# Optimization experiments

Measured on AMD Instinct MI355X. Metric: run time of the kernel, lower is better.

Reference implementation:

```python
import jax, jax.numpy as jnp
import numpy as np

B, C, H, W = 32, 256, 7, 7
HEADS = 8
DIM_HEAD = 64
INNER = HEADS * DIM_HEAD  # 512
N_ANGLES = 16
KS = 5
GROUPS = 32
EPS = 1e-5


def setup_inputs() -> dict:
    key = jax.random.key(0)
    ks = jax.random.split(key, 16)
    w = lambda k, shp: jax.random.normal(k, shp, jnp.float32) * 0.05
    return {
        'x': jax.random.normal(ks[0], (B, C, H, W), jnp.float32),
        'gn_g': jnp.ones((C,), jnp.float32), 'gn_b': jnp.zeros((C,), jnp.float32),
        'sa_w1': w(ks[1], (C // 8, C)), 'sa_b1': jnp.zeros((C // 8,), jnp.float32),
        'sa_w2': w(ks[2], (C, C // 8)), 'sa_b2': jnp.zeros((C,), jnp.float32),
        'sa_gn_g': jnp.ones((C,), jnp.float32), 'sa_gn_b': jnp.zeros((C,), jnp.float32),
        'ra_gn_g': jnp.ones((C,), jnp.float32), 'ra_gn_b': jnp.zeros((C,), jnp.float32),
        'ra_qkv_w': w(ks[3], (3 * C, C)),
        'ra_proj_w': w(ks[4], (C, C)), 'ra_proj_b': jnp.zeros((C,), jnp.float32),
        'aa_ln_g': jnp.ones((C,), jnp.float32), 'aa_ln_b': jnp.zeros((C,), jnp.float32),
        'aa_qkv_w': w(ks[5], (3 * INNER, C)),
        'aa_relpos': w(ks[6], (2 * 7 - 1, 2 * 7 - 1, HEADS)),
        'aa_out_w': w(ks[7], (C, INNER)), 'aa_out_b': jnp.zeros((C,), jnp.float32),
        'ad_dir_w': w(ks[8], (N_ANGLES, C, C, KS, KS)),
        'ad_ap_w1': w(ks[9], (128, C)), 'ad_ap_b1': jnp.zeros((128,), jnp.float32),
        'ad_ap_w2': w(ks[10], (N_ANGLES, 128)), 'ad_ap_b2': jnp.zeros((N_ANGLES,), jnp.float32),
        'ad_proj_w': w(ks[11], (C, C)), 'ad_proj_b': jnp.zeros((C,), jnp.float32),
        'gate_w': w(ks[12], (4, C)), 'gate_b': jnp.zeros((4,), jnp.float32),
        'proj_w': w(ks[13], (C, C)), 'proj_b': jnp.zeros((C,), jnp.float32),
    }


def _gn(x, g, b):
    Bx, Cx, Hx, Wx = x.shape
    xr = x.reshape(Bx, GROUPS, -1)
    m = xr.mean(-1, keepdims=True)
    v = xr.var(-1, keepdims=True)
    xn = ((xr - m) * jax.lax.rsqrt(v + EPS)).reshape(Bx, Cx, Hx, Wx)
    return xn * g[None, :, None, None] + b[None, :, None, None]


def _c1(x, w, b=None):
    y = jnp.einsum('bchw,oc->bohw', x, w)
    return y if b is None else y + b[None, :, None, None]


def _rot_attn_pass(x, qkv_w):
    Bx, Cx, Hx, Wx = x.shape
    d = Cx // HEADS
    q, k, v = jnp.split(_c1(x, qkv_w), 3, axis=1)
    sh = lambda t: t.reshape(Bx, HEADS, d, Hx * Wx).transpose(0, 1, 3, 2)  # b h n d
    q, k, v = sh(q), sh(k), sh(v)
    a = jax.nn.softmax(jnp.einsum('bhid,bhjd->bhij', q, k) * (d ** -0.5), axis=-1)
    o = jnp.einsum('bhij,bhjd->bhid', a, v)
    return o.transpose(0, 1, 3, 2).reshape(Bx, Cx, Hx, Wx)


def _forward(x, gn_g, gn_b, sa_w1, sa_b1, sa_w2, sa_b2, sa_gn_g, sa_gn_b,
             ra_gn_g, ra_gn_b, ra_qkv_w, ra_proj_w, ra_proj_b,
             aa_ln_g, aa_ln_b, aa_qkv_w, aa_relpos, aa_out_w, aa_out_b,
             ad_dir_w, ad_ap_w1, ad_ap_b1, ad_ap_w2, ad_ap_b2, ad_proj_w, ad_proj_b,
             gate_w, gate_b, proj_w, proj_b):
    normed = _gn(x, gn_g, gn_b)

    # --- SpatialAttention branch ---
    wts = jax.nn.sigmoid(_c1(jax.nn.relu(_c1(normed, sa_w1, sa_b1)), sa_w2, sa_b2))
    spatial = _gn(normed * wts + normed, sa_gn_g, sa_gn_b)

    # --- RotationAwareAttention branch: 4 rot90 passes, max-fused ---
    xr = _gn(normed, ra_gn_g, ra_gn_b)
    r0 = _rot_attn_pass(xr, ra_qkv_w)
    r1 = jnp.rot90(_rot_attn_pass(jnp.rot90(xr, 1, (2, 3)), ra_qkv_w), 3, (2, 3))
    r2 = jnp.rot90(_rot_attn_pass(jnp.rot90(xr, 2, (2, 3)), ra_qkv_w), 2, (2, 3))
    r3 = jnp.rot90(_rot_attn_pass(jnp.rot90(xr, 3, (2, 3)), ra_qkv_w), 1, (2, 3))
    mx = jnp.maximum(jnp.maximum(r0, r1), jnp.maximum(r2, r3))
    rotation = _c1(mx, ra_proj_w, ra_proj_b) + normed

    # --- AngleAwareSelfAttention branch (rel-pos-biased MHSA over 49 tokens) ---
    Nn = H * W
    t = normed.reshape(B, C, Nn).transpose(0, 2, 1)  # [B,N,C]
    mu = t.mean(-1, keepdims=True)
    var = t.var(-1, keepdims=True)
    tn = (t - mu) * jax.lax.rsqrt(var + EPS) * aa_ln_g + aa_ln_b
    q, k, v = jnp.split(jnp.einsum('bnc,oc->bno', tn, aa_qkv_w), 3, axis=-1)
    sh = lambda u: u.reshape(B, Nn, HEADS, DIM_HEAD).transpose(0, 2, 1, 3)
    q, k, v = sh(q), sh(k), sh(v)
    dots = jnp.einsum('bhid,bhjd->bhij', q, k) * (DIM_HEAD ** -0.5)
    idx = jnp.arange(Nn)
    yi, xi = idx // W, idx % W
    dy = yi[None, :] - yi[:, None] + (H - 1)  # offsets into 13x13 table
    dx = xi[None, :] - xi[:, None] + (W - 1)
    bias = aa_relpos[dy, dx].transpose(2, 0, 1)[None]  # [1,heads,N,N]
    attn = jax.nn.softmax(dots + bias, axis=-1)
    o = jnp.einsum('bhij,bhjd->bhid', attn, v).transpose(0, 2, 1, 3).reshape(B, Nn, INNER)
    o = jnp.einsum('bni,oi->bno', o, aa_out_w) + aa_out_b
    angle = o.transpose(0, 2, 1).reshape(B, C, H, W) + normed

    # --- AngleAdaptiveAttention branch: 16 directional 5x5 convs + learned softmax gate ---
    dir_out = jax.lax.conv_general_dilated(
        normed, ad_dir_w.reshape(N_ANGLES * C, C, KS, KS), (1, 1), 'SAME',
        dimension_numbers=('NCHW', 'OIHW', 'NCHW')).reshape(B, N_ANGLES, C, H, W)
    gap = normed.mean((2, 3))  # [B,C]
    h1 = jax.nn.relu(gap @ ad_ap_w1.T + ad_ap_b1)
    aw = jax.nn.softmax(h1 @ ad_ap_w2.T + ad_ap_b2, axis=1)  # [B,16]
    comb = jnp.einsum('bkchw,bk->bchw', dir_out, aw)
    adaptive = _c1(comb, ad_proj_w, ad_proj_b) + normed

    # --- gated fusion ---
    gates = jax.nn.softmax(_c1(x, gate_w, gate_b), axis=1)  # [B,4,H,W]
    fused = (spatial * gates[:, 0:1] + rotation * gates[:, 1:2]
             + angle * gates[:, 2:3] + adaptive * gates[:, 3:4])
    return _c1(fused, proj_w, proj_b) + x


def reference(x, gn_g, gn_b, sa_w1, sa_b1, sa_w2, sa_b2, sa_gn_g, sa_gn_b,
              ra_gn_g, ra_gn_b, ra_qkv_w, ra_proj_w, ra_proj_b,
              aa_ln_g, aa_ln_b, aa_qkv_w, aa_relpos, aa_out_w, aa_out_b,
              ad_dir_w, ad_ap_w1, ad_ap_b1, ad_ap_w2, ad_ap_b2, ad_proj_w, ad_proj_b,
              gate_w, gate_b, proj_w, proj_b):
    return _forward(x, gn_g, gn_b, sa_w1, sa_b1, sa_w2, sa_b2, sa_gn_g, sa_gn_b,
                    ra_gn_g, ra_gn_b, ra_qkv_w, ra_proj_w, ra_proj_b,
                    aa_ln_g, aa_ln_b, aa_qkv_w, aa_relpos, aa_out_w, aa_out_b,
                    ad_dir_w, ad_ap_w1, ad_ap_b1, ad_ap_w2, ad_ap_b2, ad_proj_w, ad_proj_b,
                    gate_w, gate_b, proj_w, proj_b)
```

## Files before the change

kernel.cpp:

```cpp
#include <hip/hip_runtime.h>

#define EPS 1e-5f
typedef unsigned short u16;
typedef unsigned int u32;
typedef float f32x4 __attribute__((ext_vector_type(4)));
typedef short bf16x8 __attribute__((ext_vector_type(8)));

__device__ __forceinline__ float bf2f(u16 h){
  return __uint_as_float(((u32)h) << 16);
}
__device__ __forceinline__ u16 f2bf(float f){
  u32 u = __float_as_uint(f);
  u += 0x7fffu + ((u >> 16) & 1u);
  return (u16)(u >> 16);
}
__device__ __forceinline__ u32 pk2(float lo, float hi){
  return ((u32)f2bf(hi) << 16) | (u32)f2bf(lo);
}
union BF8 { bf16x8 v; u32 u[4]; };

__global__ __launch_bounds__(256) void k_prep1(
    const float* __restrict__ x, const float* __restrict__ gn_g, const float* __restrict__ gn_b,
    const float* __restrict__ ra_g, const float* __restrict__ ra_b,
    float* __restrict__ normed, float* __restrict__ xr, float* __restrict__ gap)
{
  int ch = blockIdx.x, b = blockIdx.y;
  int c0 = ch * 32;
  __shared__ float xs[1568], ns[1568];
  const float* xb = x + ((size_t)b * 256 + c0) * 49;
  for (int i = threadIdx.x; i < 1568; i += 256) xs[i] = xb[i];
  __syncthreads();
  int wv = threadIdx.x >> 6, lane = threadIdx.x & 63;
  const float* gsrc = xs + wv * 392;
  float* ndst = ns + wv * 392;
  float s = 0.f, ss = 0.f;
  for (int i = lane; i < 392; i += 64){ float v = gsrc[i]; s += v; ss += v * v; }
  for (int off = 32; off; off >>= 1){ s += __shfl_down(s, off); ss += __shfl_down(ss, off); }
  s = __shfl(s, 0); ss = __shfl(ss, 0);
  float m = s / 392.f, rs = rsqrtf(ss / 392.f - m * m + EPS);
  for (int i = lane; i < 392; i += 64){
    int c = c0 + wv * 8 + i / 49;
    ndst[i] = (gsrc[i] - m) * rs * gn_g[c] + gn_b[c];
  }
  __syncthreads();
  float* nb = normed + ((size_t)b * 256 + c0) * 49;
  for (int i = threadIdx.x; i < 1568; i += 256) nb[i] = ns[i];
  if (threadIdx.x < 32){
    float g2 = 0.f; const float* rp = ns + threadIdx.x * 49;
    for (int p = 0; p < 49; p++) g2 += rp[p];
    gap[(size_t)b * 256 + c0 + threadIdx.x] = g2 * (1.f / 49.f);
  }
  s = 0.f; ss = 0.f;
  for (int i = lane; i < 392; i += 64){ float v = ndst[i]; s += v; ss += v * v; }
  for (int off = 32; off; off >>= 1){ s += __shfl_down(s, off); ss += __shfl_down(ss, off); }
  s = __shfl(s, 0); ss = __shfl(ss, 0);
  m = s / 392.f; rs = rsqrtf(ss / 392.f - m * m + EPS);
  float* xrb = xr + ((size_t)b * 256 + c0) * 49;
  for (int i = lane; i < 392; i += 64){
    int c = c0 + wv * 8 + i / 49;
    xrb[wv * 392 + i] = (ndst[i] - m) * rs * ra_g[c] + ra_b[c];
  }
}

__global__ __launch_bounds__(256) void k_pos(
    const float* __restrict__ x, const float* __restrict__ normed,
    const float* __restrict__ gate_w, const float* __restrict__ gate_b,
    float* __restrict__ gates_g, float* __restrict__ lnm_g, float* __restrict__ lnr_g)
{
  int pc = blockIdx.x, b = blockIdx.y;
  __shared__ float gw[1024];
  for (int i = threadIdx.x; i < 1024; i += 256) gw[i] = gate_w[i];
  __syncthreads();
  int wv = threadIdx.x >> 6, lane = threadIdx.x & 63;
  for (int pi = wv; pi < 7; pi += 4){
    int p = pc * 7 + pi;
    const float* nb = normed + (size_t)b * 12544 + p;
    const float* xb = x + (size_t)b * 12544 + p;
    float s = 0.f, ss = 0.f, g0 = 0.f, g1 = 0.f, g2 = 0.f, g3 = 0.f;
    for (int c = lane; c < 256; c += 64){
      float nv = nb[c * 49];
      float xv = xb[c * 49];
      s += nv; ss += nv * nv;
      g0 += xv * gw[c]; g1 += xv * gw[256 + c];
      g2 += xv * gw[512 + c]; g3 += xv * gw[768 + c];
    }
    for (int off = 32; off; off >>= 1){
      s += __shfl_down(s, off); ss += __shfl_down(ss, off);
      g0 += __shfl_down(g0, off); g1 += __shfl_down(g1, off);
      g2 += __shfl_down(g2, off); g3 += __shfl_down(g3, off);
    }
    if (lane == 0){
      float mu = s / 256.f;
      lnm_g[b * 49 + p] = mu;
      lnr_g[b * 49 + p] = rsqrtf(ss / 256.f - mu * mu + EPS);
      g0 += gate_b[0]; g1 += gate_b[1]; g2 += gate_b[2]; g3 += gate_b[3];
      float mx = fmaxf(fmaxf(g0, g1), fmaxf(g2, g3));
      float e0 = __expf(g0 - mx), e1 = __expf(g1 - mx), e2 = __expf(g2 - mx), e3 = __expf(g3 - mx);
      float inv = 1.f / (e0 + e1 + e2 + e3);
      float* gg = gates_g + (size_t)b * 196 + p;
      gg[0] = e0 * inv; gg[49] = e1 * inv; gg[98] = e2 * inv; gg[147] = e3 * inv;
    }
  }
}

__global__ __launch_bounds__(256) void k_h1aw(
    const float* __restrict__ normed, const float* __restrict__ sa_w1, const float* __restrict__ sa_b1,
    const float* __restrict__ ap_w1, const float* __restrict__ ap_b1,
    const float* __restrict__ ap_w2, const float* __restrict__ ap_b2,
    const float* __restrict__ gap_g,
    float* __restrict__ h1_g, float* __restrict__ aw_g)
{
  int xb2 = blockIdx.x, b = blockIdx.y;
  int t = threadIdx.x;
  if (xb2 == 7){
    __shared__ float gaps[256], h[128], lg[16];
    gaps[t] = gap_g[b * 256 + t];
    __syncthreads();
    if (t < 128){
      float s = ap_b1[t];
      const float* wr = ap_w1 + t * 256;
      #pragma unroll 4
      for (int c = 0; c < 256; c++) s += gaps[c] * wr[c];
      h[t] = fmaxf(s, 0.f);
    }
    __syncthreads();
    if (t < 16){
      float s = ap_b2[t];
      const float* wr = ap_w2 + t * 128;
      #pragma unroll 4
      for (int o = 0; o < 128; o++) s += h[o] * wr[o];
      lg[t] = s;
    }
    __syncthreads();
    if (t == 0){
      float mx = -1e30f;
      for (int k = 0; k < 16; k++) mx = fmaxf(mx, lg[k]);
      float e[16], sm = 0.f;
      for (int k = 0; k < 16; k++){ e[k] = __expf(lg[k] - mx); sm += e[k]; }
      float inv = 1.f / sm;
      for (int k = 0; k < 16; k++) aw_g[b * 16 + k] = e[k] * inv;
    }
    return;
  }
  __shared__ float w1t[256 * 33];
  __shared__ float ns2[256 * 7];
  int p0 = xb2 * 7;
  for (int i = t; i < 8192; i += 256){
    int o = i >> 8, c = i & 255;
    w1t[c * 33 + o] = sa_w1[i];
  }
  for (int i = t; i < 1792; i += 256){
    int c = i / 7, pl = i - c * 7;
    ns2[i] = normed[(size_t)b * 12544 + c * 49 + p0 + pl];
  }
  __syncthreads();
  if (t < 224){
    int pl = t >> 5, o = t & 31;
    float s = sa_b1[o];
    #pragma unroll 8
    for (int c = 0; c < 256; c++) s += ns2[c * 7 + pl] * w1t[c * 33 + o];
    h1_g[(size_t)b * 1568 + (p0 + pl) * 32 + o] = fmaxf(s, 0.f);
  }
}

__global__ __launch_bounds__(256) void k_spatial(
    const float* __restrict__ normed, const float* __restrict__ h1_g,
    const float* __restrict__ sa_w2, const float* __restrict__ sa_b2,
    const float* __restrict__ sa_g, const float* __restrict__ sa_bb,
    float* __restrict__ spat_g)
{
  int gc = blockIdx.x, b = blockIdx.y;
  __shared__ float h1s[49 * 33];
  __shared__ float w2s[1024];
  int t = threadIdx.x;
  for (int i = t; i < 1568; i += 256){
    int p = i >> 5, o = i & 31;
    h1s[p * 33 + o] = h1_g[(size_t)b * 1568 + i];
  }
  for (int i = t; i < 1024; i += 256) w2s[i] = sa_w2[gc * 1024 + i];
  __syncthreads();
  int wv = t >> 6, lane = t & 63;
  int cg0 = wv * 8;
  const float* nb = normed + (size_t)b * 12544 + (gc * 32 + cg0) * 49;
  float tmp[7];
  float s = 0.f, ss = 0.f;
  #pragma unroll
  for (int j = 0; j < 7; j++){
    int i = lane + 64 * j;
    float v = 0.f;
    if (i < 392){
      int c = i / 49;
      const float* wr = w2s + (cg0 + c) * 32;
      const float* hp = h1s + (i - c * 49) * 33;
      float d = sa_b2[gc * 32 + cg0 + c];
      #pragma unroll
      for (int o = 0; o < 32; o++) d += hp[o] * wr[o];
      v = nb[i] * (1.f + 1.f / (1.f + __expf(-d)));
      s += v; ss += v * v;
    }
    tmp[j] = v;
  }
  for (int off = 32; off; off >>= 1){ s += __shfl_down(s, off); ss += __shfl_down(ss, off); }
  s = __shfl(s, 0); ss = __shfl(ss, 0);
  float m = s / 392.f, rs = rsqrtf(ss / 392.f - m * m + EPS);
  float* sb = spat_g + (size_t)b * 12544 + (gc * 32 + cg0) * 49;
  #pragma unroll
  for (int j = 0; j < 7; j++){
    int i = lane + 64 * j;
    if (i < 392){
      int c = gc * 32 + cg0 + i / 49;
      sb[i] = (tmp[j] - m) * rs * sa_g[c] + sa_bb[c];
    }
  }
}

__global__ __launch_bounds__(256) void k_weff(
    const float* __restrict__ W, const float* __restrict__ aw, u16* __restrict__ weff)
{
  const size_t t = ((size_t)blockIdx.x * 256 + threadIdx.x) * 2;
  const size_t CS = 819200;
  float2 A[16], B[16];
  #pragma unroll
  for (int k = 0; k < 16; k++) A[k] = *(const float2*)(W + (size_t)k * 1638400 + t);
  #pragma unroll
  for (int k = 0; k < 16; k++) B[k] = *(const float2*)(W + (size_t)k * 1638400 + t + CS);

  #pragma unroll 1
  for (int b = 0; b < 32; b++){
    float s0 = 0.f, s1 = 0.f;
    #pragma unroll
    for (int k = 0; k < 16; k++){
      float a = aw[b * 16 + k];
      s0 += a * A[k].x; s1 += a * A[k].y;
    }
    __builtin_nontemporal_store(pk2(s0, s1), (u32*)(weff + (size_t)b * 1638400 + t));
  }
  #pragma unroll 1
  for (int b = 0; b < 32; b++){
    float s0 = 0.f, s1 = 0.f;
    #pragma unroll
    for (int k = 0; k < 16; k++){
      float a = aw[b * 16 + k];
      s0 += a * B[k].x; s1 += a * B[k].y;
    }
    __builtin_nontemporal_store(pk2(s0, s1), (u32*)(weff + (size_t)b * 1638400 + t + CS));
  }
}

__global__ __launch_bounds__(256) void k_im2col(
    const float* __restrict__ normed, u16* __restrict__ xim)
{
  int p = blockIdx.x, b = blockIdx.y;
  __shared__ u16 row[6400];
  int ci = threadIdx.x;
  int py = p / 7, px = p - py * 7;
  const float* nb = normed + (size_t)b * 12544 + ci * 49;
  u16* rp = row + ci * 25;
  #pragma unroll
  for (int sy = 0; sy < 5; sy++){
    int iy = py + sy - 2;
    #pragma unroll
    for (int sx = 0; sx < 5; sx++){
      int ix = px + sx - 2;
      float v = (iy >= 0 && iy < 7 && ix >= 0 && ix < 7) ? nb[iy * 7 + ix] : 0.f;
      rp[sy * 5 + sx] = f2bf(v);
    }
  }
  __syncthreads();
  const u32* rs = (const u32*)row;
  u32* od = (u32*)(xim + (size_t)(b * 49 + p) * 6400);
  for (int i = threadIdx.x; i < 3200; i += 256) od[i] = rs[i];
}

__global__ __launch_bounds__(256) void k_conv_mfma(
    const u16* __restrict__ weff, const u16* __restrict__ xim, float* __restrict__ partial)
{
  int bx = blockIdx.x, b = blockIdx.y;
  int mblk = bx >> 3, kp = bx & 7;
  int wv = threadIdx.x >> 6, lane = threadIdx.x & 63;
  int lo = lane & 15, hi = lane >> 4;
  int co0 = mblk * 128 + wv * 32;
  const u16* wr0 = weff + (size_t)b * 1638400 + (size_t)(co0 + lo) * 6400 + kp * 800 + hi * 8;
  const u16* wr1 = wr0 + 16 * 6400;
  const u16* xb = xim + (size_t)b * 313600 + (size_t)lo * 6400 + kp * 800 + hi * 8;
  f32x4 acc[2][4];
  #pragma unroll
  for (int mi = 0; mi < 2; mi++)
    #pragma unroll
    for (int pi = 0; pi < 4; pi++) acc[mi][pi] = (f32x4){0.f, 0.f, 0.f, 0.f};
  #pragma unroll 1
  for (int ks = 0; ks < 25; ks++){
    int k0 = ks * 32;
    bf16x8 A0 = *(const bf16x8*)(wr0 + k0);
    bf16x8 A1 = *(const bf16x8*)(wr1 + k0);
    bf16x8 B0 = *(const bf16x8*)(xb + k0);
    bf16x8 B1 = *(const bf16x8*)(xb + 16 * 6400 + k0);
    bf16x8 B2 = *(const bf16x8*)(xb + 32 * 6400 + k0);
    bf16x8 B3 = *(const bf16x8*)(xb + 48 * 6400 + k0);
    acc[0][0] = __builtin_amdgcn_mfma_f32_16x16x32_bf16(A0, B0, acc[0][0], 0, 0, 0);
    acc[0][1] = __builtin_amdgcn_mfma_f32_16x16x32_bf16(A0, B1, acc[0][1], 0, 0, 0);
    acc[0][2] = __builtin_amdgcn_mfma_f32_16x16x32_bf16(A0, B2, acc[0][2], 0, 0, 0);
    acc[0][3] = __builtin_amdgcn_mfma_f32_16x16x32_bf16(A0, B3, acc[0][3], 0, 0, 0);
    acc[1][0] = __builtin_amdgcn_mfma_f32_16x16x32_bf16(A1, B0, acc[1][0], 0, 0, 0);
    acc[1][1] = __builtin_amdgcn_mfma_f32_16x16x32_bf16(A1, B1, acc[1][1], 0, 0, 0);
    acc[1][2] = __builtin_amdgcn_mfma_f32_16x16x32_bf16(A1, B2, acc[1][2], 0, 0, 0);
    acc[1][3] = __builtin_amdgcn_mfma_f32_16x16x32_bf16(A1, B3, acc[1][3], 0, 0, 0);
  }
  float* pb = partial + ((size_t)kp * 32 + b) * 12544;
  #pragma unroll
  for (int mi = 0; mi < 2; mi++){
    #pragma unroll
    for (int pi = 0; pi < 4; pi++){
      int p = pi * 16 + lo;
      if (p < 49){
        #pragma unroll
        for (int r = 0; r < 4; r++){
          int co = co0 + mi * 16 + hi * 4 + r;
          pb[co * 49 + p] = acc[mi][pi][r];
        }
      }
    }
  }
}

__global__ __launch_bounds__(256) void k_conv_reduce(
    const float* __restrict__ part, float* __restrict__ comb)
{
  int i = blockIdx.x * 256 + threadIdx.x;
  if (i >= 100352) return;
  float a0 = 0.f, a1 = 0.f, a2 = 0.f, a3 = 0.f;
  #pragma unroll
  for (int p = 0; p < 8; p++){
    float4 v = ((const float4*)part)[(size_t)p * 100352 + i];
    a0 += v.x; a1 += v.y; a2 += v.z; a3 += v.w;
  }
  float4 o; o.x = a0; o.y = a1; o.z = a2; o.w = a3;
  ((float4*)comb)[i] = o;
}

__device__ __forceinline__ void mfma_gemm_dev(
    const float* __restrict__ W, const float* __restrict__ bias,
    const float* __restrict__ act, const float* __restrict__ res,
    float* __restrict__ out, int M, int K, int m0blk, int p0, int b,
    const float* __restrict__ lnm, const float* __restrict__ lnr,
    const float* __restrict__ lng, const float* __restrict__ lnb)
{
  int wv = threadIdx.x >> 6, lane = threadIdx.x & 63;
  int lo = lane & 15, hi = lane >> 4;
  int m0 = m0blk + wv * 32;
  int p = p0 + lo;
  bool pok = p < 49;
  const float* ab = act + (size_t)b * K * 49;
  float lm = 0.f, lr = 0.f;
  if (lng && pok){ lm = lnm[p]; lr = lnr[p]; }
  f32x4 acc0 = {0.f, 0.f, 0.f, 0.f};
  f32x4 acc1 = {0.f, 0.f, 0.f, 0.f};
  const float* wr0 = W + (size_t)(m0 + lo) * K + hi * 8;
  const float* wr1 = W + (size_t)(m0 + 16 + lo) * K + hi * 8;
  for (int k0 = 0; k0 < K; k0 += 32){
    int kb = k0 + hi * 8;
    float4 a0lo = *(const float4*)(wr0 + k0);
    float4 a0hi = *(const float4*)(wr0 + k0 + 4);
    float4 a1lo = *(const float4*)(wr1 + k0);
    float4 a1hi = *(const float4*)(wr1 + k0 + 4);
    float bv[8];
    if (pok){
      const float* ap = ab + (size_t)kb * 49 + p;
      #pragma unroll
      for (int i = 0; i < 8; i++) bv[i] = ap[i * 49];
      if (lng){
// ... 1 lines not shown
        for (int i = 0; i < 8; i++) bv[i] = (bv[i] - lm) * lr * lng[kb + i] + lnb[kb + i];
      }
    } else {
      #pragma unroll
      for (int i = 0; i < 8; i++) bv[i] = 0.f;
    }
    BF8 A0, A1, B;
    A0.u[0] = pk2(a0lo.x, a0lo.y); A0.u[1] = pk2(a0lo.z, a0lo.w);
    A0.u[2] = pk2(a0hi.x, a0hi.y); A0.u[3] = pk2(a0hi.z, a0hi.w);
    A1.u[0] = pk2(a1lo.x, a1lo.y); A1.u[1] = pk2(a1lo.z, a1lo.w);
    A1.u[2] = pk2(a1hi.x, a1hi.y); A1.u[3] = pk2(a1hi.z, a1hi.w);
    B.u[0] = pk2(bv[0], bv[1]); B.u[1] = pk2(bv[2], bv[3]);
    B.u[2] = pk2(bv[4], bv[5]); B.u[3] = pk2(bv[6], bv[7]);
    acc0 = __builtin_amdgcn_mfma_f32_16x16x32_bf16(A0.v, B.v, acc0, 0, 0, 0);
    acc1 = __builtin_amdgcn_mfma_f32_16x16x32_bf16(A1.v, B.v, acc1, 0, 0, 0);
  }
  if (pok){
    #pragma unroll
    for (int r = 0; r < 4; r++){
      int m = m0 + hi * 4 + r;
      size_t idx = ((size_t)b * M + m) * 49 + p;
      float v = acc0[r] + (bias ? bias[m] : 0.f);
      if (res) v += res[idx];
      out[idx] = v;
      int m2 = m + 16;
      size_t idx2 = idx + 16 * 49;
      float v2 = acc1[r] + (bias ? bias[m2] : 0.f);
      if (res) v2 += res[idx2];
      out[idx2] = v2;
    }
  }
}

__global__ __launch_bounds__(256) void k_qkv(
    const float* __restrict__ ra_w, const float* __restrict__ aa_w,
    const float* __restrict__ xr, const float* __restrict__ normed,
    const float* __restrict__ lnm, const float* __restrict__ lnr,
    const float* __restrict__ ln_g, const float* __restrict__ ln_b,
    float* __restrict__ ra_qkv, float* __restrict__ aa_qkv)
{
  int bx = blockIdx.x, b = blockIdx.y;
  if (bx < 24){
    int m0 = (bx >> 2) * 128, p0 = (bx & 3) * 16;
    mfma_gemm_dev(ra_w, nullptr, xr, nullptr, ra_qkv, 768, 256, m0, p0, b,
                  nullptr, nullptr, nullptr, nullptr);
  } else {
    int bx2 = bx - 24;
    int m0 = (bx2 >> 2) * 128, p0 = (bx2 & 3) * 16;
    mfma_gemm_dev(aa_w, nullptr, normed, nullptr, aa_qkv, 1536, 256, m0, p0, b,
                  lnm + b * 49, lnr + b * 49, ln_g, ln_b);
  }
}

__global__ __launch_bounds__(256) void k_proj3(
    const float* __restrict__ ra_pw, const float* __restrict__ ra_pb, const float* __restrict__ r0,
    const float* __restrict__ aa_ow, const float* __restrict__ aa_ob, const float* __restrict__ aa_o,
    const float* __restrict__ ad_pw, const float* __restrict__ ad_pb, const float* __restrict__ comb,
    const float* __restrict__ normed,
    float* __restrict__ rotf, float* __restrict__ angf, float* __restrict__ adpf)
{
  int bx = blockIdx.x, b = blockIdx.y;
  if (bx < 8){
    int m0 = (bx >> 2) * 128, p0 = (bx & 3) * 16;
    mfma_gemm_dev(ra_pw, ra_pb, r0, normed, rotf, 256, 256, m0, p0, b,
                  nullptr, nullptr, nullptr, nullptr);
  } else if (bx < 16){
    int bx2 = bx - 8;
    int m0 = (bx2 >> 2) * 128, p0 = (bx2 & 3) * 16;
    mfma_gemm_dev(aa_ow, aa_ob, aa_o, normed, angf, 256, 512, m0, p0, b,
                  nullptr, nullptr, nullptr, nullptr);
  } else {
    int bx2 = bx - 16;
    int m0 = (bx2 >> 2) * 128, p0 = (bx2 & 3) * 16;
    mfma_gemm_dev(ad_pw, ad_pb, comb, normed, adpf, 256, 256, m0, p0, b,
                  nullptr, nullptr, nullptr, nullptr);
  }
}

__global__ __launch_bounds__(256) void k_final(
    const float* __restrict__ proj_w, const float* __restrict__ proj_b,
    const float* __restrict__ spat, const float* __restrict__ rotf,
    const float* __restrict__ angf, const float* __restrict__ adpf,
    const float* __restrict__ gates, const float* __restrict__ x,
    float* __restrict__ out)
// ... 22 lines not shown
    float4 a1lo = *(const float4*)(wr1 + k0);
    float4 a1hi = *(const float4*)(wr1 + k0 + 4);
    float bv[8];
    if (pok){
      size_t base = boff + (size_t)kb * 49 + p;
      #pragma unroll
      for (int i = 0; i < 8; i++){
        size_t idx = base + (size_t)i * 49;
        bv[i] = spat[idx] * g0 + rotf[idx] * g1 + angf[idx] * g2 + adpf[idx] * g3;
      }
    } else {
      #pragma unroll
      for (int i = 0; i < 8; i++) bv[i] = 0.f;
    }
    BF8 A0, A1, B;
    A0.u[0] = pk2(a0lo.x, a0lo.y); A0.u[1] = pk2(a0lo.z, a0lo.w);
    A0.u[2] = pk2(a0hi.x, a0hi.y); A0.u[3] = pk2(a0hi.z, a0hi.w);
    A1.u[0] = pk2(a1lo.x, a1lo.y); A1.u[1] = pk2(a1lo.z, a1lo.w);
    A1.u[2] = pk2(a1hi.x, a1hi.y); A1.u[3] = pk2(a1hi.z, a1hi.w);
    B.u[0] = pk2(bv[0], bv[1]); B.u[1] = pk2(bv[2], bv[3]);
    B.u[2] = pk2(bv[4], bv[5]); B.u[3] = pk2(bv[6], bv[7]);
    acc0 = __builtin_amdgcn_mfma_f32_16x16x32_bf16(A0.v, B.v, acc0, 0, 0, 0);
    acc1 = __builtin_amdgcn_mfma_f32_16x16x32_bf16(A1.v, B.v, acc1, 0, 0, 0);
  }
  if (pok){
    #pragma unroll
    for (int r = 0; r < 4; r++){
      int m = m0 + hi * 4 + r;
      size_t idx = boff + (size_t)m * 49 + p;
      out[idx] = acc0[r] + proj_b[m] + x[idx];
      int m2 = m + 16;
      size_t idx2 = idx + 16 * 49;
      out[idx2] = acc1[r] + proj_b[m2] + x[idx2];
    }
  }
}

__device__ __forceinline__ void softmax_rows(float* sc, int tid)
{
  int r = tid >> 2, q = tid & 3;
  if (r < 49){
    float* row = sc + r * 52;
    float mx = -1e30f;
    for (int j = q; j < 49; j += 4) mx = fmaxf(mx, row[j]);
    mx = fmaxf(mx, __shfl_xor(mx, 1));
    mx = fmaxf(mx, __shfl_xor(mx, 2));
    float sm = 0.f;
    for (int j = q; j < 49; j += 4){ float e = __expf(row[j] - mx); row[j] = e; sm += e; }
    sm += __shfl_xor(sm, 1);
    sm += __shfl_xor(sm, 2);
    float inv = 1.f / sm;
    for (int j = q; j < 49; j += 4) row[j] *= inv;
  }
}

__global__ __launch_bounds__(256) void k_attn(
    const float* __restrict__ ra_qkv, const float* __restrict__ aa_qkv,
    const float* __restrict__ relpos,
    float* __restrict__ r0, float* __restrict__ ao)
{
  __shared__ float sm[3 * 49 * 65 + 49 * 52];
  int xb2 = blockIdx.x, b = blockIdx.y;
  if (xb2 < 8){
    int hd = xb2;
    float* qs = sm; float* ks = sm + 1617; float* vs = sm + 3234; float* sc = sm + 4851;
    const float* base = ra_qkv + (size_t)b * 768 * 49;
    for (int i = threadIdx.x; i < 1568; i += 256){
      int d = i / 49, tok = i - d * 49;
      qs[tok * 33 + d] = base[(hd * 32 + d) * 49 + tok];
      ks[tok * 33 + d] = base[(256 + hd * 32 + d) * 49 + tok];
      vs[tok * 33 + d] = base[(512 + hd * 32 + d) * 49 + tok];
    }
    __syncthreads();
    const float scale = 0.17677669529663687f;
    for (int it = threadIdx.x; it < 2401; it += 256){
      int i = it / 49, j = it - i * 49;
      float s = 0.f;
      #pragma unroll
      for (int d = 0; d < 32; d++) s += qs[i * 33 + d] * ks[j * 33 + d];
      sc[i * 52 + j] = s * scale;
    }
    __syncthreads();
    softmax_rows(sc, threadIdx.x);
    __syncthreads();
    for (int it = threadIdx.x; it < 1568; it += 256){
      int d = it / 49, i = it - d * 49;
      float o = 0.f;
      for (int j = 0; j < 49; j++) o += sc[i * 52 + j] * vs[j * 33 + d];
      r0[((size_t)b * 256 + hd * 32 + d) * 49 + i] = o;
    }
  } else {
    int hd = xb2 - 8;
    float* qs = sm; float* ks = sm + 3185; float* vs = sm + 6370; float* sc = sm + 9555;
    const float* base = aa_qkv + (size_t)b * 1536 * 49;
    for (int i = threadIdx.x; i < 3136; i += 256){
      int d = i / 49, tok = i - d * 49;
      qs[tok * 65 + d] = base[(hd * 64 + d) * 49 + tok];
      ks[tok * 65 + d] = base[(512 + hd * 64 + d) * 49 + tok];
      vs[tok * 65 + d] = base[(1024 + hd * 64 + d) * 49 + tok];
    }
    __syncthreads();
    for (int it = threadIdx.x; it < 2401; it += 256){
      int i = it / 49, j = it - i * 49;
      float s = 0.f;
      #pragma unroll
      for (int d = 0; d < 64; d++) s += qs[i * 65 + d] * ks[j * 65 + d];
      int dy = j / 7 - i / 7 + 6, dx = j % 7 - i % 7 + 6;
      sc[i * 52 + j] = s * 0.125f + relpos[(dy * 13 + dx) * 8 + hd];
    }
    __syncthreads();
    softmax_rows(sc, threadIdx.x);
    __syncthreads();
    for (int it = threadIdx.x; it < 3136; it += 256){
      int d = it / 49, i = it - d * 49;
      float o = 0.f;
      for (int j = 0; j < 49; j++) o += sc[i * 52 + j] * vs[j * 65 + d];
      ao[((size_t)b * 512 + hd * 64 + d) * 49 + i] = o;
    }
  }
}

extern "C" void kernel_launch(void* const* d_in, const int* in_sizes, int n_in,
                              void* d_out, int out_size, void* d_ws, size_t ws_size,
                              hipStream_t stream)
{
  const float* x        = (const float*)d_in[0];
  const float* gn_g     = (const float*)d_in[1];
  const float* gn_b     = (const float*)d_in[2];
  const float* sa_w1    = (const float*)d_in[3];
  const float* sa_b1    = (const float*)d_in[4];
  const float* sa_w2    = (const float*)d_in[5];
  const float* sa_b2    = (const float*)d_in[6];
  const float* sa_gn_g  = (const float*)d_in[7];
  const float* sa_gn_b  = (const float*)d_in[8];
  const float* ra_gn_g  = (const float*)d_in[9];
  const float* ra_gn_b  = (const float*)d_in[10];
  const float* ra_qkv_w = (const float*)d_in[11];
  const float* ra_proj_w= (const float*)d_in[12];
  const float* ra_proj_b= (const float*)d_in[13];
  const float* aa_ln_g  = (const float*)d_in[14];
  const float* aa_ln_b  = (const float*)d_in[15];
  const float* aa_qkv_w = (const float*)d_in[16];
  const float* aa_relpos= (const float*)d_in[17];
  const float* aa_out_w = (const float*)d_in[18];
  const float* aa_out_b = (const float*)d_in[19];
  const float* ad_dir_w = (const float*)d_in[20];
  const float* ad_ap_w1 = (const float*)d_in[21];
  const float* ad_ap_b1 = (const float*)d_in[22];
  const float* ad_ap_w2 = (const float*)d_in[23];
  const float* ad_ap_b2 = (const float*)d_in[24];
  const float* ad_proj_w= (const float*)d_in[25];
  const float* ad_proj_b= (const float*)d_in[26];
  const float* gate_w   = (const float*)d_in[27];
  const float* gate_b   = (const float*)d_in[28];
  const float* proj_w   = (const float*)d_in[29];
  const float* proj_b   = (const float*)d_in[30];

  char* ws = (char*)d_ws;
  float* normed    = (float*)(ws + 0);
  float* xr        = (float*)(ws + 1605632);
  float* h1_g      = (float*)(ws + 3211264);
  float* lnm       = (float*)(ws + 3420160);
  float* lnr       = (float*)(ws + 3426560);
  float* spatial   = (float*)(ws + 4816896);
  float* rotf      = (float*)(ws + 6422528);
  float* anglef    = (float*)(ws + 8028160);
  float* adaptf    = (float*)(ws + 9633792);
  float* r0        = (float*)(ws + 12845056);
  float* gap       = (float*)(ws + 14450688);
  float* aw        = (float*)(ws + 14483456);
  float* gates     = (float*)(ws + 14485504);
  float* ra_qkv    = (float*)(ws + 14510592);
  float* aa_qkv    = (float*)(ws + 19327488);
  float* aa_o      = (float*)(ws + 28961280);
  float* comb      = (float*)(ws + 32172544);
  float* partial   = (float*)(ws + 33778176);
  u16*   xim       = (u16*)  (ws + 46623232);
  u16*   weff      = (u16*)  (ws + 66693632);

  float* out = (float*)d_out;

  k_prep1<<<dim3(8, 32), 256, 0, stream>>>(x, gn_g, gn_b, ra_gn_g, ra_gn_b, normed, xr, gap);
  k_pos<<<dim3(7, 32), 256, 0, stream>>>(x, normed, gate_w, gate_b, gates, lnm, lnr);
  k_h1aw<<<dim3(8, 32), 256, 0, stream>>>(normed, sa_w1, sa_b1,
                                          ad_ap_w1, ad_ap_b1, ad_ap_w2, ad_ap_b2,
                                          gap, h1_g, aw);
  k_spatial<<<dim3(8, 32), 256, 0, stream>>>(normed, h1_g, sa_w2, sa_b2, sa_gn_g, sa_gn_b, spatial);
  k_weff<<<dim3(1600), 256, 0, stream>>>(ad_dir_w, aw, weff);
  k_im2col<<<dim3(49, 32), 256, 0, stream>>>(normed, xim);
  k_qkv<<<dim3(72, 32), 256, 0, stream>>>(ra_qkv_w, aa_qkv_w, xr, normed,
                                          lnm, lnr, aa_ln_g, aa_ln_b, ra_qkv, aa_qkv);
  k_attn<<<dim3(16, 32), 256, 0, stream>>>(ra_qkv, aa_qkv, aa_relpos, r0, aa_o);
  k_conv_mfma<<<dim3(16, 32), 256, 0, stream>>>(weff, xim, partial);
  k_conv_reduce<<<dim3(392), 256, 0, stream>>>(partial, comb);
  k_proj3<<<dim3(24, 32), 256, 0, stream>>>(ra_proj_w, ra_proj_b, r0,
                                            aa_out_w, aa_out_b, aa_o,
                                            ad_proj_w, ad_proj_b, comb,
                                            normed, rotf, anglef, adaptf);
  k_final<<<dim3(8, 32), 256, 0, stream>>>(proj_w, proj_b, spatial, rotf, anglef, adaptf,
                                           gates, x, out);
}
```

Baseline: 291.1 us.

## Merge independent stages into combined kernels to cut launches and overlap work

Folds independent stages into shared launches: gates/LN stats with the SA hidden layer and angle weights; weff with QKV GEMMs, im2col and spatial; conv MFMA with both attention passes. Blocks pick their stage from a linear block id, so stages with no data dependence can run on the GPU at the same time and launch gaps go away. The weff computation now handles 4 elements per thread with float4 loads instead of two float2 halves, and the conv weight loads become nontemporal. The risk is block imbalance inside each mega-kernel and higher shared memory per block, since each kernel reserves the largest buffer any of its stages needs.

```diff
diff --git a/kernel.cpp b/kernel.cpp
--- a/kernel.cpp
+++ b/kernel.cpp
@@ -5,6 +5,7 @@
 typedef unsigned int u32;
 typedef float f32x4 __attribute__((ext_vector_type(4)));
 typedef short bf16x8 __attribute__((ext_vector_type(8)));
+typedef unsigned int u32x2 __attribute__((ext_vector_type(2)));
 
 __device__ __forceinline__ float bf2f(u16 h){
   return __uint_as_float(((u32)h) << 16);
@@ -62,13 +63,13 @@
   }
 }
 
-__global__ __launch_bounds__(256) void k_pos(
+__device__ void dev_pos(
     const float* __restrict__ x, const float* __restrict__ normed,
     const float* __restrict__ gate_w, const float* __restrict__ gate_b,
-    float* __restrict__ gates_g, float* __restrict__ lnm_g, float* __restrict__ lnr_g)
-{
-  int pc = blockIdx.x, b = blockIdx.y;
-  __shared__ float gw[1024];
+    float* __restrict__ gates_g, float* __restrict__ lnm_g, float* __restrict__ lnr_g,
+    int pc, int b, float* sm)
+{
+  float* gw = sm;
   for (int i = threadIdx.x; i < 1024; i += 256) gw[i] = gate_w[i];
   __syncthreads();
   int wv = threadIdx.x >> 6, lane = threadIdx.x & 63;
@@ -103,17 +104,17 @@
   }
 }
 
-__global__ __launch_bounds__(256) void k_h1aw(
+__device__ void dev_h1aw(
     const float* __restrict__ normed, const float* __restrict__ sa_w1, const float* __restrict__ sa_b1,
     const float* __restrict__ ap_w1, const float* __restrict__ ap_b1,
     const float* __restrict__ ap_w2, const float* __restrict__ ap_b2,
     const float* __restrict__ gap_g,
-    float* __restrict__ h1_g, float* __restrict__ aw_g)
-{
-  int xb2 = blockIdx.x, b = blockIdx.y;
+    float* __restrict__ h1_g, float* __restrict__ aw_g,
+    int xb2, int b, float* sm)
+{
   int t = threadIdx.x;
   if (xb2 == 7){
-    __shared__ float gaps[256], h[128], lg[16];
+    float* gaps = sm; float* h = sm + 256; float* lg = sm + 384;
     gaps[t] = gap_g[b * 256 + t];
     __syncthreads();
     if (t < 128){
@@ -135,15 +136,15 @@
     if (t == 0){
       float mx = -1e30f;
       for (int k = 0; k < 16; k++) mx = fmaxf(mx, lg[k]);
-      float e[16], sm = 0.f;
-      for (int k = 0; k < 16; k++){ e[k] = __expf(lg[k] - mx); sm += e[k]; }
-      float inv = 1.f / sm;
+      float e[16], smm = 0.f;
+      for (int k = 0; k < 16; k++){ e[k] = __expf(lg[k] - mx); smm += e[k]; }
+      float inv = 1.f / smm;
       for (int k = 0; k < 16; k++) aw_g[b * 16 + k] = e[k] * inv;
     }
     return;
   }
-  __shared__ float w1t[256 * 33];
-  __shared__ float ns2[256 * 7];
+  float* w1t = sm;
+  float* ns2 = sm + 8448;
   int p0 = xb2 * 7;
   for (int i = t; i < 8192; i += 256){
     int o = i >> 8, c = i & 255;
@@ -163,15 +164,32 @@
   }
 }
 
-__global__ __launch_bounds__(256) void k_spatial(
+__global__ __launch_bounds__(256) void k_pre2(
+    const float* __restrict__ x, const float* __restrict__ normed,
+    const float* __restrict__ gate_w, const float* __restrict__ gate_b,
+    const float* __restrict__ sa_w1, const float* __restrict__ sa_b1,
+    const float* __restrict__ ap_w1, const float* __restrict__ ap_b1,
+    const float* __restrict__ ap_w2, const float* __restrict__ ap_b2,
+    const float* __restrict__ gap_g,
+    float* __restrict__ gates_g, float* __restrict__ lnm_g, float* __restrict__ lnr_g,
+    float* __restrict__ h1_g, float* __restrict__ aw_g)
+{
+  __shared__ float sm[10240];
+  int bx = blockIdx.x, b = blockIdx.y;
+  if (bx < 7)
+    dev_pos(x, normed, gate_w, gate_b, gates_g, lnm_g, lnr_g, bx, b, sm);
+  else
+    dev_h1aw(normed, sa_w1, sa_b1, ap_w1, ap_b1, ap_w2, ap_b2, gap_g, h1_g, aw_g, bx - 7, b, sm);
+}
+
+__device__ void dev_spatial(
     const float* __restrict__ normed, const float* __restrict__ h1_g,
     const float* __restrict__ sa_w2, const float* __restrict__ sa_b2,
     const float* __restrict__ sa_g, const float* __restrict__ sa_bb,
-    float* __restrict__ spat_g)
-{
-  int gc = blockIdx.x, b = blockIdx.y;
-  __shared__ float h1s[49 * 33];
-  __shared__ float w2s[1024];
+    float* __restrict__ spat_g, int gc, int b, float* sm)
+{
+  float* h1s = sm;
+  float* w2s = sm + 1617;
   int t = threadIdx.x;
   for (int i = t; i < 1568; i += 256){
     int p = i >> 5, o = i & 31;
@@ -214,44 +232,30 @@
   }
 }
 
-__global__ __launch_bounds__(256) void k_weff(
-    const float* __restrict__ W, const float* __restrict__ aw, u16* __restrict__ weff)
-{
-  const size_t t = ((size_t)blockIdx.x * 256 + threadIdx.x) * 2;
-  const size_t CS = 819200;
-  float2 A[16], B[16];
+__device__ void dev_weff(
+    const float* __restrict__ W, const float* __restrict__ aw, u16* __restrict__ weff, int bx)
+{
+  const size_t t = ((size_t)bx * 256 + threadIdx.x) * 4;
+  float4 A[16];
   #pragma unroll
-  for (int k = 0; k < 16; k++) A[k] = *(const float2*)(W + (size_t)k * 1638400 + t);
-  #pragma unroll
-  for (int k = 0; k < 16; k++) B[k] = *(const float2*)(W + (size_t)k * 1638400 + t + CS);
-
+  for (int k = 0; k < 16; k++) A[k] = *(const float4*)(W + (size_t)k * 1638400 + t);
   #pragma unroll 1
   for (int b = 0; b < 32; b++){
-    float s0 = 0.f, s1 = 0.f;
+    float s0 = 0.f, s1 = 0.f, s2 = 0.f, s3 = 0.f;
     #pragma unroll
     for (int k = 0; k < 16; k++){
       float a = aw[b * 16 + k];
-      s0 += a * A[k].x; s1 += a * A[k].y;
-    }
-    __builtin_nontemporal_store(pk2(s0, s1), (u32*)(weff + (size_t)b * 1638400 + t));
-  }
-  #pragma unroll 1
-  for (int b = 0; b < 32; b++){
-    float s0 = 0.f, s1 = 0.f;
-    #pragma unroll
-    for (int k = 0; k < 16; k++){
-      float a = aw[b * 16 + k];
-      s0 += a * B[k].x; s1 += a * B[k].y;
-    }
-    __builtin_nontemporal_store(pk2(s0, s1), (u32*)(weff + (size_t)b * 1638400 + t + CS));
-  }
-}
-
-__global__ __launch_bounds__(256) void k_im2col(
-    const float* __restrict__ normed, u16* __restrict__ xim)
-{
-  int p = blockIdx.x, b = blockIdx.y;
-  __shared__ u16 row[6400];
+      s0 += a * A[k].x; s1 += a * A[k].y; s2 += a * A[k].z; s3 += a * A[k].w;
+    }
+    u32x2 o; o.x = pk2(s0, s1); o.y = pk2(s2, s3);
+    __builtin_nontemporal_store(o, (u32x2*)(weff + (size_t)b * 1638400 + t));
+  }
+}
+
+__device__ void dev_im2col(
+    const float* __restrict__ normed, u16* __restrict__ xim, int p, int b, float* sm)
+{
+  u16* row = (u16*)sm;
   int ci = threadIdx.x;
   int py = p / 7, px = p - py * 7;
   const float* nb = normed + (size_t)b * 12544 + ci * 49;
@@ -270,72 +274,6 @@
   const u32* rs = (const u32*)row;
   u32* od = (u32*)(xim + (size_t)(b * 49 + p) * 6400);
   for (int i = threadIdx.x; i < 3200; i += 256) od[i] = rs[i];
-}
-
-__global__ __launch_bounds__(256) void k_conv_mfma(
-    const u16* __restrict__ weff, const u16* __restrict__ xim, float* __restrict__ partial)
-{
-  int bx = blockIdx.x, b = blockIdx.y;
-  int mblk = bx >> 3, kp = bx & 7;
-  int wv = threadIdx.x >> 6, lane = threadIdx.x & 63;
-  int lo = lane & 15, hi = lane >> 4;
-  int co0 = mblk * 128 + wv * 32;
-  const u16* wr0 = weff + (size_t)b * 1638400 + (size_t)(co0 + lo) * 6400 + kp * 800 + hi * 8;
-  const u16* wr1 = wr0 + 16 * 6400;
-  const u16* xb = xim + (size_t)b * 313600 + (size_t)lo * 6400 + kp * 800 + hi * 8;
-  f32x4 acc[2][4];
-  #pragma unroll
-  for (int mi = 0; mi < 2; mi++)
-    #pragma unroll
-    for (int pi = 0; pi < 4; pi++) acc[mi][pi] = (f32x4){0.f, 0.f, 0.f, 0.f};
-  #pragma unroll 1
-  for (int ks = 0; ks < 25; ks++){
-    int k0 = ks * 32;
-    bf16x8 A0 = *(const bf16x8*)(wr0 + k0);
-    bf16x8 A1 = *(const bf16x8*)(wr1 + k0);
-    bf16x8 B0 = *(const bf16x8*)(xb + k0);
-    bf16x8 B1 = *(const bf16x8*)(xb + 16 * 6400 + k0);
-    bf16x8 B2 = *(const bf16x8*)(xb + 32 * 6400 + k0);
-    bf16x8 B3 = *(const bf16x8*)(xb + 48 * 6400 + k0);
-    acc[0][0] = __builtin_amdgcn_mfma_f32_16x16x32_bf16(A0, B0, acc[0][0], 0, 0, 0);
-    acc[0][1] = __builtin_amdgcn_mfma_f32_16x16x32_bf16(A0, B1, acc[0][1], 0, 0, 0);
-    acc[0][2] = __builtin_amdgcn_mfma_f32_16x16x32_bf16(A0, B2, acc[0][2], 0, 0, 0);
-    acc[0][3] = __builtin_amdgcn_mfma_f32_16x16x32_bf16(A0, B3, acc[0][3], 0, 0, 0);
-    acc[1][0] = __builtin_amdgcn_mfma_f32_16x16x32_bf16(A1, B0, acc[1][0], 0, 0, 0);
-    acc[1][1] = __builtin_amdgcn_mfma_f32_16x16x32_bf16(A1, B1, acc[1][1], 0, 0, 0);
-    acc[1][2] = __builtin_amdgcn_mfma_f32_16x16x32_bf16(A1, B2, acc[1][2], 0, 0, 0);
-    acc[1][3] = __builtin_amdgcn_mfma_f32_16x16x32_bf16(A1, B3, acc[1][3], 0, 0, 0);
-  }
-  float* pb = partial + ((size_t)kp * 32 + b) * 12544;
-  #pragma unroll
-  for (int mi = 0; mi < 2; mi++){
-    #pragma unroll
-    for (int pi = 0; pi < 4; pi++){
-      int p = pi * 16 + lo;
-      if (p < 49){
-        #pragma unroll
-        for (int r = 0; r < 4; r++){
-          int co = co0 + mi * 16 + hi * 4 + r;
-          pb[co * 49 + p] = acc[mi][pi][r];
-        }
-      }
-    }
-  }
-}
-
-__global__ __launch_bounds__(256) void k_conv_reduce(
-    const float* __restrict__ part, float* __restrict__ comb)
-{
-  int i = blockIdx.x * 256 + threadIdx.x;
-  if (i >= 100352) return;
-  float a0 = 0.f, a1 = 0.f, a2 = 0.f, a3 = 0.f;
-  #pragma unroll
-  for (int p = 0; p < 8; p++){
-    float4 v = ((const float4*)part)[(size_t)p * 100352 + i];
-    a0 += v.x; a1 += v.y; a2 += v.z; a3 += v.w;
-  }
-  float4 o; o.x = a0; o.y = a1; o.z = a2; o.w = a3;
-  ((float4*)comb)[i] = o;
 }
 
 __device__ __forceinline__ void mfma_gemm_dev(
@@ -403,24 +341,205 @@
   }
 }
 
-__global__ __launch_bounds__(256) void k_qkv(
+__global__ __launch_bounds__(256) void k_mega1(
+    const float* __restrict__ ad_dir_w, const float* __restrict__ aw, u16* __restrict__ weff,
     const float* __restrict__ ra_w, const float* __restrict__ aa_w,
     const float* __restrict__ xr, const float* __restrict__ normed,
     const float* __restrict__ lnm, const float* __restrict__ lnr,
     const float* __restrict__ ln_g, const float* __restrict__ ln_b,
-    float* __restrict__ ra_qkv, float* __restrict__ aa_qkv)
-{
-  int bx = blockIdx.x, b = blockIdx.y;
-  if (bx < 24){
-    int m0 = (bx >> 2) * 128, p0 = (bx & 3) * 16;
-    mfma_gemm_dev(ra_w, nullptr, xr, nullptr, ra_qkv, 768, 256, m0, p0, b,
-                  nullptr, nullptr, nullptr, nullptr);
+    float* __restrict__ ra_qkv, float* __restrict__ aa_qkv,
+    u16* __restrict__ xim,
+    const float* __restrict__ h1_g, const float* __restrict__ sa_w2, const float* __restrict__ sa_b2,
+    const float* __restrict__ sa_g, const float* __restrict__ sa_bb, float* __restrict__ spat_g)
+{
+  __shared__ float sm[3300];
+  int id = blockIdx.x;
+  if (id < 1600){
+    dev_weff(ad_dir_w, aw, weff, id);
+  } else if (id < 3904){
+    int q = id - 1600;
+    int bx = q % 72, b = q / 72;
+    if (bx < 24){
+      int m0 = (bx >> 2) * 128, p0 = (bx & 3) * 16;
+      mfma_gemm_dev(ra_w, nullptr, xr, nullptr, ra_qkv, 768, 256, m0, p0, b,
+                    nullptr, nullptr, nullptr, nullptr);
+    } else {
+      int bx2 = bx - 24;
+      int m0 = (bx2 >> 2) * 128, p0 = (bx2 & 3) * 16;
+      mfma_gemm_dev(aa_w, nullptr, normed, nullptr, aa_qkv, 1536, 256, m0, p0, b,
+                    lnm + b * 49, lnr + b * 49, ln_g, ln_b);
+    }
+  } else if (id < 5472){
+    int q = id - 3904;
+    dev_im2col(normed, xim, q % 49, q / 49, sm);
   } else {
-    int bx2 = bx - 24;
-    int m0 = (bx2 >> 2) * 128, p0 = (bx2 & 3) * 16;
-    mfma_gemm_dev(aa_w, nullptr, normed, nullptr, aa_qkv, 1536, 256, m0, p0, b,
-                  lnm + b * 49, lnr + b * 49, ln_g, ln_b);
-  }
+    int q = id - 5472;
+    dev_spatial(normed, h1_g, sa_w2, sa_b2, sa_g, sa_bb, spat_g, q % 8, q / 8, sm);
+  }
+}
+
+__device__ void dev_conv(
+    const u16* __restrict__ weff, const u16* __restrict__ xim, float* __restrict__ partial,
+    int bx, int b)
+{
+  int mblk = bx >> 3, kp = bx & 7;
+  int wv = threadIdx.x >> 6, lane = threadIdx.x & 63;
+  int lo = lane & 15, hi = lane >> 4;
+  int co0 = mblk * 128 + wv * 32;
+  const u16* wr0 = weff + (size_t)b * 1638400 + (size_t)(co0 + lo) * 6400 + kp * 800 + hi * 8;
+  const u16* wr1 = wr0 + 16 * 6400;
+  const u16* xb = xim + (size_t)b * 313600 + (size_t)lo * 6400 + kp * 800 + hi * 8;
+  f32x4 acc[2][4];
+  #pragma unroll
+  for (int mi = 0; mi < 2; mi++)
+    #pragma unroll
+    for (int pi = 0; pi < 4; pi++) acc[mi][pi] = (f32x4){0.f, 0.f, 0.f, 0.f};
+  #pragma unroll 1
+  for (int ks = 0; ks < 25; ks++){
+    int k0 = ks * 32;
+    bf16x8 A0 = __builtin_nontemporal_load((const bf16x8*)(wr0 + k0));
+    bf16x8 A1 = __builtin_nontemporal_load((const bf16x8*)(wr1 + k0));
+    bf16x8 B0 = *(const bf16x8*)(xb + k0);
+    bf16x8 B1 = *(const bf16x8*)(xb + 16 * 6400 + k0);
+    bf16x8 B2 = *(const bf16x8*)(xb + 32 * 6400 + k0);
+    bf16x8 B3 = *(const bf16x8*)(xb + 48 * 6400 + k0);
+    acc[0][0] = __builtin_amdgcn_mfma_f32_16x16x32_bf16(A0, B0, acc[0][0], 0, 0, 0);
+    acc[0][1] = __builtin_amdgcn_mfma_f32_16x16x32_bf16(A0, B1, acc[0][1], 0, 0, 0);
+    acc[0][2] = __builtin_amdgcn_mfma_f32_16x16x32_bf16(A0, B2, acc[0][2], 0, 0, 0);
+    acc[0][3] = __builtin_amdgcn_mfma_f32_16x16x32_bf16(A0, B3, acc[0][3], 0, 0, 0);
+    acc[1][0] = __builtin_amdgcn_mfma_f32_16x16x32_bf16(A1, B0, acc[1][0], 0, 0, 0);
+    acc[1][1] = __builtin_amdgcn_mfma_f32_16x16x32_bf16(A1, B1, acc[1][1], 0, 0, 0);
+    acc[1][2] = __builtin_amdgcn_mfma_f32_16x16x32_bf16(A1, B2, acc[1][2], 0, 0, 0);
+    acc[1][3] = __builtin_amdgcn_mfma_f32_16x16x32_bf16(A1, B3, acc[1][3], 0, 0, 0);
+  }
+  float* pb = partial + ((size_t)kp * 32 + b) * 12544;
+  #pragma unroll
+  for (int mi = 0; mi < 2; mi++){
+    #pragma unroll
+    for (int pi = 0; pi < 4; pi++){
+      int p = pi * 16 + lo;
+      if (p < 49){
+        #pragma unroll
+        for (int r = 0; r < 4; r++){
+          int co = co0 + mi * 16 + hi * 4 + r;
+          pb[co * 49 + p] = acc[mi][pi][r];
+        }
+      }
+    }
+  }
+}
+
+__device__ __forceinline__ void softmax_rows(float* sc, int tid)
+{
+  int r = tid >> 2, q = tid & 3;
+  if (r < 49){
+    float* row = sc + r * 52;
+    float mx = -1e30f;
+    for (int j = q; j < 49; j += 4) mx = fmaxf(mx, row[j]);
+    mx = fmaxf(mx, __shfl_xor(mx, 1));
+    mx = fmaxf(mx, __shfl_xor(mx, 2));
+    float sm = 0.f;
+    for (int j = q; j < 49; j += 4){ float e = __expf(row[j] - mx); row[j] = e; sm += e; }
+    sm += __shfl_xor(sm, 1);
+    sm += __shfl_xor(sm, 2);
+    float inv = 1.f / sm;
+    for (int j = q; j < 49; j += 4) row[j] *= inv;
+  }
+}
+
+__device__ void dev_attn(
+    const float* __restrict__ ra_qkv, const float* __restrict__ aa_qkv,
+    const float* __restrict__ relpos,
+    float* __restrict__ r0, float* __restrict__ ao,
+    int xb2, int b, float* sm)
+{
+  if (xb2 < 8){
+    int hd = xb2;
+    float* qs = sm; float* ks = sm + 1617; float* vs = sm + 3234; float* sc = sm + 4851;
+    const float* base = ra_qkv + (size_t)b * 768 * 49;
+    for (int i = threadIdx.x; i < 1568; i += 256){
+      int d = i / 49, tok = i - d * 49;
+      qs[tok * 33 + d] = base[(hd * 32 + d) * 49 + tok];
+      ks[tok * 33 + d] = base[(256 + hd * 32 + d) * 49 + tok];
+      vs[tok * 33 + d] = base[(512 + hd * 32 + d) * 49 + tok];
+    }
+    __syncthreads();
+    const float scale = 0.17677669529663687f;
+    for (int it = threadIdx.x; it < 2401; it += 256){
+      int i = it / 49, j = it - i * 49;
+      float s = 0.f;
+      #pragma unroll
+      for (int d = 0; d < 32; d++) s += qs[i * 33 + d] * ks[j * 33 + d];
+      sc[i * 52 + j] = s * scale;
+    }
+    __syncthreads();
+    softmax_rows(sc, threadIdx.x);
+    __syncthreads();
+    for (int it = threadIdx.x; it < 1568; it += 256){
+      int d = it / 49, i = it - d * 49;
+      float o = 0.f;
+      for (int j = 0; j < 49; j++) o += sc[i * 52 + j] * vs[j * 33 + d];
+      r0[((size_t)b * 256 + hd * 32 + d) * 49 + i] = o;
+    }
+  } else {
+    int hd = xb2 - 8;
+    float* qs = sm; float* ks = sm + 3185; float* vs = sm + 6370; float* sc = sm + 9555;
+    const float* base = aa_qkv + (size_t)b * 1536 * 49;
+    for (int i = threadIdx.x; i < 3136; i += 256){
+      int d = i / 49, tok = i - d * 49;
+      qs[tok * 65 + d] = base[(hd * 64 + d) * 49 + tok];
+      ks[tok * 65 + d] = base[(512 + hd * 64 + d) * 49 + tok];
+      vs[tok * 65 + d] = base[(1024 + hd * 64 + d) * 49 + tok];
+    }
+    __syncthreads();
+    for (int it = threadIdx.x; it < 2401; it += 256){
+      int i = it / 49, j = it - i * 49;
+      float s = 0.f;
+      #pragma unroll
+      for (int d = 0; d < 64; d++) s += qs[i * 65 + d] * ks[j * 65 + d];
+      int dy = j / 7 - i / 7 + 6, dx = j % 7 - i % 7 + 6;
+      sc[i * 52 + j] = s * 0.125f + relpos[(dy * 13 + dx) * 8 + hd];
+    }
+    __syncthreads();
+    softmax_rows(sc, threadIdx.x);
+    __syncthreads();
+    for (int it = threadIdx.x; it < 3136; it += 256){
+      int d = it / 49, i = it - d * 49;
+      float o = 0.f;
+      for (int j = 0; j < 49; j++) o += sc[i * 52 + j] * vs[j * 65 + d];
+      ao[((size_t)b * 512 + hd * 64 + d) * 49 + i] = o;
+    }
+  }
+}
+
+__global__ __launch_bounds__(256) void k_mega2(
+    const u16* __restrict__ weff, const u16* __restrict__ xim, float* __restrict__ partial,
+    const float* __restrict__ ra_qkv, const float* __restrict__ aa_qkv,
+    const float* __restrict__ relpos, float* __restrict__ r0, float* __restrict__ ao)
+{
+  __shared__ float sm[12103];
+  int id = blockIdx.x;
+  if (id < 512){
+    dev_conv(weff, xim, partial, id % 16, id / 16);
+  } else {
+    int q = id - 512;
+    dev_attn(ra_qkv, aa_qkv, relpos, r0, ao, q % 16, q / 16, sm);
+  }
+}
+
+__global__ __launch_bounds__(256) void k_conv_reduce(
+    const float* __restrict__ part, float* __restrict__ comb)
+{
+  int i = blockIdx.x * 256 + threadIdx.x;
+  if (i >= 100352) return;
+  float a0 = 0.f, a1 = 0.f, a2 = 0.f, a3 = 0.f;
+  #pragma unroll
+  for (int p = 0; p < 8; p++){
+    float4 v = ((const float4*)part)[(size_t)p * 100352 + i];
+    a0 += v.x; a1 += v.y; a2 += v.z; a3 += v.w;
+  }
+  float4 o; o.x = a0; o.y = a1; o.z = a2; o.w = a3;
+  ((float4*)comb)[i] = o;
 }
 
 __global__ __launch_bounds__(256) void k_proj3(
@@ -509,90 +628,6 @@
       int m2 = m + 16;
       size_t idx2 = idx + 16 * 49;
       out[idx2] = acc1[r] + proj_b[m2] + x[idx2];
-    }
-  }
-}
-
-__device__ __forceinline__ void softmax_rows(float* sc, int tid)
-{
-  int r = tid >> 2, q = tid & 3;
-  if (r < 49){
-    float* row = sc + r * 52;
-    float mx = -1e30f;
-    for (int j = q; j < 49; j += 4) mx = fmaxf(mx, row[j]);
-    mx = fmaxf(mx, __shfl_xor(mx, 1));
-    mx = fmaxf(mx, __shfl_xor(mx, 2));
-    float sm = 0.f;
-    for (int j = q; j < 49; j += 4){ float e = __expf(row[j] - mx); row[j] = e; sm += e; }
-    sm += __shfl_xor(sm, 1);
-    sm += __shfl_xor(sm, 2);
-    float inv = 1.f / sm;
-    for (int j = q; j < 49; j += 4) row[j] *= inv;
-  }
-}
-
-__global__ __launch_bounds__(256) void k_attn(
-    const float* __restrict__ ra_qkv, const float* __restrict__ aa_qkv,
-    const float* __restrict__ relpos,
-    float* __restrict__ r0, float* __restrict__ ao)
-{
-  __shared__ float sm[3 * 49 * 65 + 49 * 52];
-  int xb2 = blockIdx.x, b = blockIdx.y;
-  if (xb2 < 8){
-    int hd = xb2;
-    float* qs = sm; float* ks = sm + 1617; float* vs = sm + 3234; float* sc = sm + 4851;
-    const float* base = ra_qkv + (size_t)b * 768 * 49;
-    for (int i = threadIdx.x; i < 1568; i += 256){
-      int d = i / 49, tok = i - d * 49;
-      qs[tok * 33 + d] = base[(hd * 32 + d) * 49 + tok];
-      ks[tok * 33 + d] = base[(256 + hd * 32 + d) * 49 + tok];
-      vs[tok * 33 + d] = base[(512 + hd * 32 + d) * 49 + tok];
-    }
-    __syncthreads();
-    const float scale = 0.17677669529663687f;
-    for (int it = threadIdx.x; it < 2401; it += 256){
-      int i = it / 49, j = it - i * 49;
-      float s = 0.f;
-      #pragma unroll
-      for (int d = 0; d < 32; d++) s += qs[i * 33 + d] * ks[j * 33 + d];
-      sc[i * 52 + j] = s * scale;
-    }
-    __syncthreads();
-    softmax_rows(sc, threadIdx.x);
-    __syncthreads();
-    for (int it = threadIdx.x; it < 1568; it += 256){
-      int d = it / 49, i = it - d * 49;
-      float o = 0.f;
-      for (int j = 0; j < 49; j++) o += sc[i * 52 + j] * vs[j * 33 + d];
-      r0[((size_t)b * 256 + hd * 32 + d) * 49 + i] = o;
-    }
-  } else {
-    int hd = xb2 - 8;
-    float* qs = sm; float* ks = sm + 3185; float* vs = sm + 6370; float* sc = sm + 9555;
-    const float* base = aa_qkv + (size_t)b * 1536 * 49;
-    for (int i = threadIdx.x; i < 3136; i += 256){
-      int d = i / 49, tok = i - d * 49;
-      qs[tok * 65 + d] = base[(hd * 64 + d) * 49 + tok];
-      ks[tok * 65 + d] = base[(512 + hd * 64 + d) * 49 + tok];
-      vs[tok * 65 + d] = base[(1024 + hd * 64 + d) * 49 + tok];
-    }
-    __syncthreads();
-    for (int it = threadIdx.x; it < 2401; it += 256){
-      int i = it / 49, j = it - i * 49;
-      float s = 0.f;
-      #pragma unroll
-      for (int d = 0; d < 64; d++) s += qs[i * 65 + d] * ks[j * 65 + d];
-      int dy = j / 7 - i / 7 + 6, dx = j % 7 - i % 7 + 6;
-      sc[i * 52 + j] = s * 0.125f + relpos[(dy * 13 + dx) * 8 + hd];
-    }
-    __syncthreads();
-    softmax_rows(sc, threadIdx.x);
-    __syncthreads();
-    for (int it = threadIdx.x; it < 3136; it += 256){
-      int d = it / 49, i = it - d * 49;
-      float o = 0.f;
-      for (int j = 0; j < 49; j++) o += sc[i * 52 + j] * vs[j * 65 + d];
-      ao[((size_t)b * 512 + hd * 64 + d) * 49 + i] = o;
     }
   }
 }
@@ -658,17 +693,16 @@
   float* out = (float*)d_out;
 
   k_prep1<<<dim3(8, 32), 256, 0, stream>>>(x, gn_g, gn_b, ra_gn_g, ra_gn_b, normed, xr, gap);
-  k_pos<<<dim3(7, 32), 256, 0, stream>>>(x, normed, gate_w, gate_b, gates, lnm, lnr);
-  k_h1aw<<<dim3(8, 32), 256, 0, stream>>>(normed, sa_w1, sa_b1,
-                                          ad_ap_w1, ad_ap_b1, ad_ap_w2, ad_ap_b2,
-                                          gap, h1_g, aw);
-  k_spatial<<<dim3(8, 32), 256, 0, stream>>>(normed, h1_g, sa_w2, sa_b2, sa_gn_g, sa_gn_b, spatial);
-  k_weff<<<dim3(1600), 256, 0, stream>>>(ad_dir_w, aw, weff);
-  k_im2col<<<dim3(49, 32), 256, 0, stream>>>(normed, xim);
-  k_qkv<<<dim3(72, 32), 256, 0, stream>>>(ra_qkv_w, aa_qkv_w, xr, normed,
-                                          lnm, lnr, aa_ln_g, aa_ln_b, ra_qkv, aa_qkv);
-  k_attn<<<dim3(16, 32), 256, 0, stream>>>(ra_qkv, aa_qkv, aa_relpos, r0, aa_o);
-  k_conv_mfma<<<dim3(16, 32), 256, 0, stream>>>(weff, xim, partial);
+  k_pre2<<<dim3(15, 32), 256, 0, stream>>>(x, normed, gate_w, gate_b,
+                                           sa_w1, sa_b1, ad_ap_w1, ad_ap_b1, ad_ap_w2, ad_ap_b2,
+                                           gap, gates, lnm, lnr, h1_g, aw);
+  k_mega1<<<dim3(5728), 256, 0, stream>>>(ad_dir_w, aw, weff,
+                                          ra_qkv_w, aa_qkv_w, xr, normed,
+                                          lnm, lnr, aa_ln_g, aa_ln_b, ra_qkv, aa_qkv,
+                                          xim,
+                                          h1_g, sa_w2, sa_b2, sa_gn_g, sa_gn_b, spatial);
+  k_mega2<<<dim3(1024), 256, 0, stream>>>(weff, xim, partial,
+                                          ra_qkv, aa_qkv, aa_relpos, r0, aa_o);
   k_conv_reduce<<<dim3(392), 256, 0, stream>>>(partial, comb);
   k_proj3<<<dim3(24, 32), 256, 0, stream>>>(ra_proj_w, ra_proj_b, r0,
                                             aa_out_w, aa_out_b, aa_o,
```

After: 265.7 us. 1.1x faster.
